# Kernel optimization log

Measured on AMD Instinct MI355X. Metric: run time of the kernel, lower is better.

## Reference

```python
import jax, jax.numpy as jnp
import numpy as np

B, T, D = 4, 2048, 1024
H, KD, VD = 16, 64, 64  # num_heads, key_dim, value_dim; H*KD == D


def setup_inputs() -> dict:
    key = jax.random.key(0)
    ks = jax.random.split(key, 10)
    s = 0.02
    return {
        "q_in": jax.random.normal(ks[0], (B, T, D), jnp.float32),
        "v_in": jax.random.normal(ks[1], (B, T, D), jnp.float32),
        "Wq": jax.random.normal(ks[2], (D, H * KD), jnp.float32) * s,
        "bq": jnp.zeros((H * KD,), jnp.float32),
        "Wk": jax.random.normal(ks[3], (D, H * KD), jnp.float32) * s,
        "bk": jnp.zeros((H * KD,), jnp.float32),
        "Wv": jax.random.normal(ks[4], (D, H * VD), jnp.float32) * s,
        "bv": jnp.zeros((H * VD,), jnp.float32),
        "Wo": jax.random.normal(ks[5], (H * VD, D), jnp.float32) * s,
        "bo": jnp.zeros((D,), jnp.float32),
    }


def reference(q_in, v_in, Wq, bq, Wk, bk, Wv, bv, Wo, bo):
    # QKV projections (key defaults to value input)
    q = q_in @ Wq + bq                      # [B,T,H*KD]
    k = v_in @ Wk + bk                      # [B,T,H*KD]
    v = v_in @ Wv + bv                      # [B,T,H*VD]
    q = q.reshape(B, T, H, KD)
    k = k.reshape(B, T, H, KD)
    v = v.reshape(B, T, H, VD)
    # scaled dot-product attention, scores materialized as [B,H,Tq,Tv]
    q = q / jnp.sqrt(jnp.asarray(KD, q.dtype))
    scores = jnp.einsum('bqnh,bvnh->bnqv', q, k)
    weights = jax.nn.softmax(scores, axis=-1)
    out = jnp.einsum('bnqv,bvnh->bqnh', weights, v)  # [B,Tq,H,VD]
    out = out.reshape(B, T, H * VD)
    return out @ Wo + bo                    # [B,T,D]
```

## Files before the change

### kernel.cpp

```cpp
#include <hip/hip_runtime.h>

#define BATCH  4
#define T_SEQ  2048
#define NH     16
#define DMODEL 1024
#define HD     64

typedef float    f32x4 __attribute__((ext_vector_type(4)));
typedef _Float16 f16x8 __attribute__((ext_vector_type(8)));
typedef _Float16 f16x4 __attribute__((ext_vector_type(4)));
typedef __fp16   h16x2 __attribute__((ext_vector_type(2)));

#define LOG2E 1.44269504088896f

__device__ __forceinline__ void lds_load16(const void* g, void* l) {
  __builtin_amdgcn_global_load_lds((const __attribute__((address_space(1))) void*)g,
                                   (__attribute__((address_space(3))) void*)l, 16, 0, 0);
}

__device__ __forceinline__ f16x4 pack4_f16(float a, float b, float c, float d) {
  union { h16x2 h[2]; f16x4 f; } u;
  u.h[0] = __builtin_amdgcn_cvt_pkrtz(a, b);
  u.h[1] = __builtin_amdgcn_cvt_pkrtz(c, d);
  return u.f;
}

__global__ __launch_bounds__(256) void cast2_f32_to_f16(
    const float* __restrict__ a, const float* __restrict__ bsrc,
    _Float16* __restrict__ oa, _Float16* __restrict__ ob, int n4) {
  const float* in = blockIdx.y ? bsrc : a;
  _Float16* out = blockIdx.y ? ob : oa;
  int i = blockIdx.x * 256 + threadIdx.x;
  if (i < n4) {
    float4 v = ((const float4*)in)[i];
    f16x4 o = { (_Float16)v.x, (_Float16)v.y, (_Float16)v.z, (_Float16)v.w };
    ((f16x4*)out)[i] = o;
  }
}

__global__ __launch_bounds__(256) void transcast_w4(
    const float* __restrict__ W0, const float* __restrict__ W1,
    const float* __restrict__ W2, const float* __restrict__ W3,
    _Float16* __restrict__ T0, _Float16* __restrict__ T1,
    _Float16* __restrict__ T2, _Float16* __restrict__ T3) {
  const float* W; _Float16* Wt;
  switch (blockIdx.z) {
    case 0: W = W0; Wt = T0; break;
    case 1: W = W1; Wt = T1; break;
    case 2: W = W2; Wt = T2; break;
    default: W = W3; Wt = T3; break;
  }
  __shared__ float L[64][65];
  const int n0 = blockIdx.x * 64, k0 = blockIdx.y * 64;
  const int tx = threadIdx.x & 15, ty = threadIdx.x >> 4;
#pragma unroll
  for (int i = 0; i < 4; ++i) {
    float4 v = *(const float4*)&W[(size_t)(k0 + ty + 16 * i) * DMODEL + n0 + tx * 4];
    L[ty + 16 * i][tx * 4 + 0] = v.x;
    L[ty + 16 * i][tx * 4 + 1] = v.y;
    L[ty + 16 * i][tx * 4 + 2] = v.z;
    L[ty + 16 * i][tx * 4 + 3] = v.w;
  }
  __syncthreads();
#pragma unroll
  for (int i = 0; i < 4; ++i) {
    int n = n0 + ty + 16 * i;
    f16x4 o;
#pragma unroll
    for (int j = 0; j < 4; ++j) o[j] = (_Float16)L[tx * 4 + j][ty + 16 * i];
    *(f16x4*)&Wt[(size_t)n * DMODEL + k0 + tx * 4] = o;
  }
}

__device__ __forceinline__ void gemm_body(
    const _Float16* __restrict__ A, const _Float16* __restrict__ Wt,
    const float* __restrict__ bias, void* __restrict__ Cout, float scale,
    int mode, _Float16* As0, _Float16* Bs0, _Float16* As1, _Float16* Bs1) {
  const int K = DMODEL, N = DMODEL;
  const int tid = threadIdx.x, lane = tid & 63, wave = tid >> 6;
  const int bid = blockIdx.x + blockIdx.y * gridDim.x;
  const int m0 = ((bid & 7) * 8 + ((bid >> 3) & 7)) * 128;
  const int n0 = (bid >> 6) * 128;
  const int wm = (wave & 1) * 4, wn = (wave >> 1) * 4;
  const int m16 = lane & 15, quad = lane >> 4;

  const _Float16* ap[4]; const _Float16* bp[4];
#pragma unroll
  for (int i = 0; i < 4; ++i) {
    int gi = wave * 4 + i;
    int row = (gi >> 1) * 16 + m16;
    int kof = (gi & 1) * 32 + quad * 8;
    ap[i] = A  + (size_t)(m0 + row) * K + kof;
    bp[i] = Wt + (size_t)(n0 + row) * K + kof;
  }

  f32x4 acc[4][4] = {};

  auto stage = [&](int k0, _Float16* Asb, _Float16* Bsb) {
#pragma unroll
    for (int i = 0; i < 4; ++i) {
      lds_load16(ap[i] + k0, Asb + (wave * 4 + i) * 512);
      lds_load16(bp[i] + k0, Bsb + (wave * 4 + i) * 512);
    }
  };
  auto compute = [&](const _Float16* Asb, const _Float16* Bsb) {
#pragma unroll
    for (int s = 0; s < 2; ++s) {
      f16x8 af[4], bf[4];
#pragma unroll
      for (int t = 0; t < 4; ++t) {
        af[t] = *(const f16x8*)(Asb + (((wm + t) * 2 + s) * 64 + lane) * 8);
        bf[t] = *(const f16x8*)(Bsb + (((wn + t) * 2 + s) * 64 + lane) * 8);
      }
#pragma unroll
      for (int mi = 0; mi < 4; ++mi)
#pragma unroll
        for (int ni = 0; ni < 4; ++ni)
          acc[mi][ni] = __builtin_amdgcn_mfma_f32_16x16x32_f16(af[mi], bf[ni], acc[mi][ni], 0, 0, 0);
    }
  };

  stage(0, As0, Bs0);
  __syncthreads();
#pragma unroll
  for (int k0 = 0; k0 < 1024; k0 += 128) {
    stage(k0 + 64, As1, Bs1);
    compute(As0, Bs0);
    __syncthreads();
    if (k0 + 128 < 1024) stage(k0 + 128, As0, Bs0);
    compute(As1, Bs1);
    __syncthreads();
  }

  if (mode == 2) {
#pragma unroll
    for (int mi = 0; mi < 4; ++mi)
#pragma unroll
      for (int ni = 0; ni < 4; ++ni) {
        int row = m0 + (wm + mi) * 16 + quad * 4;
        int col = n0 + (wn + ni) * 16 + m16;
        int bb = row >> 11, tt = row & (T_SEQ - 1);
        int hh = col >> 6, dd = col & 63;
        float bv = bias[col];
        f16x4 pv = pack4_f16(acc[mi][ni][0] + bv, acc[mi][ni][1] + bv,
                             acc[mi][ni][2] + bv, acc[mi][ni][3] + bv);
        *(f16x4*)&((_Float16*)Cout)[(((size_t)bb * NH + hh) * HD + dd) * T_SEQ + tt] = pv;
      }
  } else {
#pragma unroll
    for (int mi = 0; mi < 4; ++mi)
#pragma unroll
      for (int r = 0; r < 4; ++r) {
        int row = m0 + (wm + mi) * 16 + quad * 4 + r;
#pragma unroll
        for (int ni = 0; ni < 4; ++ni) {
          int col = n0 + (wn + ni) * 16 + m16;
          float v = (acc[mi][ni][r] + bias[col]) * scale;
          if (mode == 1) ((float*)Cout)[(size_t)row * N + col] = v;
          else           ((_Float16*)Cout)[(size_t)row * N + col] = (_Float16)v;
        }
      }
  }
}

__global__ __launch_bounds__(256) void gemm_qkv(
    const _Float16* __restrict__ Aq, const _Float16* __restrict__ Av,
    const _Float16* __restrict__ Wq, const _Float16* __restrict__ Wk,
    const _Float16* __restrict__ Wv,
    const float* __restrict__ bq, const float* __restrict__ bk,
    const float* __restrict__ bv,
    _Float16* __restrict__ Cq, _Float16* __restrict__ Ck, _Float16* __restrict__ Cv) {
  __shared__ _Float16 As0[128 * 64], Bs0[128 * 64], As1[128 * 64], Bs1[128 * 64];
  const _Float16* A; const _Float16* Wt; const float* bias; _Float16* C;
  float scale; int mode;
  if (blockIdx.z == 0)      { A = Aq; Wt = Wq; bias = bq; C = Cq; scale = 0.125f * LOG2E; mode = 0; }
  else if (blockIdx.z == 1) { A = Av; Wt = Wk; bias = bk; C = Ck; scale = 1.f; mode = 0; }
  else                      { A = Av; Wt = Wv; bias = bv; C = Cv; scale = 1.f; mode = 2; }
  gemm_body(A, Wt, bias, C, scale, mode, As0, Bs0, As1, Bs1);
}

__global__ __launch_bounds__(256) void gemm_out(
    const _Float16* __restrict__ A, const _Float16* __restrict__ Wt,
    const float* __restrict__ bias, float* __restrict__ Cout) {
  __shared__ _Float16 As0[128 * 64], Bs0[128 * 64], As1[128 * 64], Bs1[128 * 64];
  gemm_body(A, Wt, bias, Cout, 1.f, 1, As0, Bs0, As1, Bs1);
}

__global__ __launch_bounds__(256) void attn_mfma(
    const _Float16* __restrict__ Q, const _Float16* __restrict__ Kb,
    const _Float16* __restrict__ Vt, _Float16* __restrict__ O) {
  __shared__ _Float16 Ks0[64 * 64], Vs0[64 * 64], Ks1[64 * 64], Vs1[64 * 64];
  __shared__ _Float16 Ps[4 * 2048];

  const int tid = threadIdx.x, lane = tid & 63, wave = tid >> 6;
  const int m16 = lane & 15, quad = lane >> 4;
  const int bidl = blockIdx.x + 16 * blockIdx.y + 256 * blockIdx.z;
  const int h = bidl & 15;
  const int q0 = ((bidl >> 4) & 15) * 128;
  const int b = bidl >> 8;
  const int wq = wave * 32;
  const int wbase = wave * 2048;

  f16x8 qf[2][2];
#pragma unroll
  for (int mi = 0; mi < 2; ++mi)
#pragma unroll
    for (int ki = 0; ki < 2; ++ki) {
      int q = q0 + wq + mi * 16 + m16;
      qf[mi][ki] = *(const f16x8*)(Q + (((size_t)b * T_SEQ + q) * NH + h) * HD + ki * 32 + quad * 8);
    }

  const _Float16 *kp[2], *vp[2];
#pragma unroll
  for (int i = 0; i < 2; ++i) {
    int g = wave * 128 + i * 64 + lane;
    int tk = (g >> 7) * 16 + (g & 15);
    int dkof = ((g >> 6) & 1) * 32 + ((g >> 4) & 3) * 8;
    kp[i] = Kb + (((size_t)b * T_SEQ + tk) * NH + h) * HD + dkof;
    int dvof = (g >> 7) * 16 + (g & 15);
    int tv = ((g >> 6) & 1) * 32 + ((g >> 4) & 3) * 8;
    vp[i] = Vt + (((size_t)b * NH + h) * HD + dvof) * T_SEQ + tv;
  }

  int pw[2][4];
#pragma unroll
  for (int mi = 0; mi < 2; ++mi)
#pragma unroll
    for (int nt = 0; nt < 4; ++nt) {
      int kt = nt >> 1;
      int q8 = ((nt & 1) << 1) | (quad >> 1);
      pw[mi][nt] = wbase + ((mi * 2 + kt) * 64 + q8 * 16 + m16) * 8 + (quad & 1) * 4;
    }

  const f16x8 onef = {(_Float16)1, (_Float16)1, (_Float16)1, (_Float16)1,
                      (_Float16)1, (_Float16)1, (_Float16)1, (_Float16)1};

  f32x4 o_acc[2][4] = {};
  f32x4 l_acc[2] = {};

  auto stageKV = [&](int kv, _Float16* Kd, _Float16* Vd) {
#pragma unroll
    for (int i = 0; i < 2; ++i) {
      lds_load16(kp[i] + (size_t)kv * (NH * HD), Kd + (wave * 2 + i) * 512);
      lds_load16(vp[i] + kv, Vd + (wave * 2 + i) * 512);
    }
  };

  auto tile = [&](const _Float16* Kd, const _Float16* Vd) {
    f32x4 st[2][4] = {};
#pragma unroll
    for (int nt = 0; nt < 4; ++nt)
#pragma unroll
      for (int ki = 0; ki < 2; ++ki) {
        f16x8 kf = *(const f16x8*)(Kd + ((nt * 2 + ki) * 64 + lane) * 8);
        st[0][nt] = __builtin_amdgcn_mfma_f32_16x16x32_f16(kf, qf[0][ki], st[0][nt], 0, 0, 0);
        st[1][nt] = __builtin_amdgcn_mfma_f32_16x16x32_f16(kf, qf[1][ki], st[1][nt], 0, 0, 0);
      }
#pragma unroll
    for (int mi = 0; mi < 2; ++mi)
#pragma unroll
      for (int nt = 0; nt < 4; ++nt) {
        f16x4 p = pack4_f16(__builtin_amdgcn_exp2f(st[mi][nt][0]),
                            __builtin_amdgcn_exp2f(st[mi][nt][1]),
                            __builtin_amdgcn_exp2f(st[mi][nt][2]),
                            __builtin_amdgcn_exp2f(st[mi][nt][3]));
        *(f16x4*)(Ps + pw[mi][nt]) = p;
      }
#pragma unroll
    for (int kt = 0; kt < 2; ++kt) {
      f16x8 pf0 = *(const f16x8*)(Ps + wbase + ((0 * 2 + kt) * 64 + lane) * 8);
      f16x8 pf1 = *(const f16x8*)(Ps + wbase + ((1 * 2 + kt) * 64 + lane) * 8);
      l_acc[0] = __builtin_amdgcn_mfma_f32_16x16x32_f16(pf0, onef, l_acc[0], 0, 0, 0);
      l_acc[1] = __builtin_amdgcn_mfma_f32_16x16x32_f16(pf1, onef, l_acc[1], 0, 0, 0);
#pragma unroll
      for (int nd = 0; nd < 4; ++nd) {
        f16x8 vf = *(const f16x8*)(Vd + ((nd * 2 + kt) * 64 + lane) * 8);
        o_acc[0][nd] = __builtin_amdgcn_mfma_f32_16x16x32_f16(pf0, vf, o_acc[0][nd], 0, 0, 0);
        o_acc[1][nd] = __builtin_amdgcn_mfma_f32_16x16x32_f16(pf1, vf, o_acc[1][nd], 0, 0, 0);
      }
    }
  };

  stageKV(0, Ks0, Vs0);
  __syncthreads();
  for (int kv = 0; kv < T_SEQ; kv += 128) {
    stageKV(kv + 64, Ks1, Vs1);
    tile(Ks0, Vs0);
    __syncthreads();
    if (kv + 128 < T_SEQ) stageKV(kv + 128, Ks0, Vs0);
    tile(Ks1, Vs1);
    __syncthreads();
  }

#pragma unroll
  for (int mi = 0; mi < 2; ++mi)
#pragma unroll
    for (int r = 0; r < 4; ++r) {
      float inv = 1.f / l_acc[mi][r];
      int q = q0 + wq + mi * 16 + quad * 4 + r;
#pragma unroll
      for (int nd = 0; nd < 4; ++nd) {
        int d = nd * 16 + m16;
        O[(((size_t)b * T_SEQ + q) * NH + h) * HD + d] = (_Float16)(o_acc[mi][nd][r] * inv);
      }
    }
}

extern "C" void kernel_launch(void* const* d_in, const int* in_sizes, int n_in,
                              void* d_out, int out_size, void* d_ws, size_t ws_size,
                              hipStream_t stream) {
  const float* q_in = (const float*)d_in[0];
  const float* v_in = (const float*)d_in[1];
  const float* Wq   = (const float*)d_in[2];
  const float* bq   = (const float*)d_in[3];
  const float* Wk   = (const float*)d_in[4];
  const float* bk   = (const float*)d_in[5];
  const float* Wv   = (const float*)d_in[6];
  const float* bv   = (const float*)d_in[7];
  const float* Wo   = (const float*)d_in[8];
  const float* bo   = (const float*)d_in[9];
  float* out = (float*)d_out;

  const size_t MB = 1u << 20;
  char* ws = (char*)d_ws;
  _Float16* q16  = (_Float16*)(ws);
  _Float16* v16  = (_Float16*)(ws + 16 * MB);
  _Float16* qbuf = (_Float16*)(ws + 32 * MB);
  _Float16* kbuf = (_Float16*)(ws + 48 * MB);
  _Float16* vtb  = (_Float16*)(ws + 64 * MB);
  _Float16* Wqt  = (_Float16*)(ws + 80 * MB);
  _Float16* Wkt  = (_Float16*)(ws + 82 * MB);
  _Float16* Wvt  = (_Float16*)(ws + 84 * MB);
  _Float16* Wot  = (_Float16*)(ws + 86 * MB);

  const int n4 = BATCH * T_SEQ * DMODEL / 4;
  cast2_f32_to_f16<<<dim3(n4 / 256, 2), 256, 0, stream>>>(q_in, v_in, q16, v16, n4);

  transcast_w4<<<dim3(16, 16, 4), 256, 0, stream>>>(Wq, Wk, Wv, Wo, Wqt, Wkt, Wvt, Wot);

  dim3 gg(DMODEL / 128, BATCH * T_SEQ / 128, 3);
  gemm_qkv<<<gg, 256, 0, stream>>>(q16, v16, Wqt, Wkt, Wvt, bq, bk, bv, qbuf, kbuf, vtb);

  attn_mfma<<<dim3(16, 16, 4), 256, 0, stream>>>(qbuf, kbuf, vtb, qbuf);

  gemm_out<<<dim3(8, 64), 256, 0, stream>>>(qbuf, Wot, bo, out);
}
```

Measured before the change: 359.3 us.

## Enlarge GEMM and attention tiles, drop double buffering for single-buffered LDS

The QKV GEMM moves to 256x128 tiles (8x4 MFMA per wave), and attention moves to 256 queries per block (64 per wave). Both reuse each staged K/V or weight tile across more rows, cutting global and LDS traffic per FLOP. All three kernels drop LDS double buffering in favour of a single buffer with two barriers per step, and launch bounds are set to raise occupancy. The trade-off is losing load/compute overlap within a block plus higher register pressure from the larger accumulators, which could cause spills or lower occupancy. Attention also runs only 512 blocks, which fills fewer CUs.

```diff
diff --git a/kernel.cpp b/kernel.cpp
--- a/kernel.cpp
+++ b/kernel.cpp
@@ -72,69 +72,59 @@
   }
 }
 
-__device__ __forceinline__ void gemm_body(
+__device__ __forceinline__ void gemm_big_body(
     const _Float16* __restrict__ A, const _Float16* __restrict__ Wt,
     const float* __restrict__ bias, void* __restrict__ Cout, float scale,
-    int mode, _Float16* As0, _Float16* Bs0, _Float16* As1, _Float16* Bs1) {
-  const int K = DMODEL, N = DMODEL;
-  const int tid = threadIdx.x, lane = tid & 63, wave = tid >> 6;
+    int mode, _Float16* As, _Float16* Bs) {
+  const int K = DMODEL;
+  const int lane = threadIdx.x & 63, wave = threadIdx.x >> 6;
   const int bid = blockIdx.x + blockIdx.y * gridDim.x;
-  const int m0 = ((bid & 7) * 8 + ((bid >> 3) & 7)) * 128;
-  const int n0 = (bid >> 6) * 128;
-  const int wm = (wave & 1) * 4, wn = (wave >> 1) * 4;
+  const int m0 = ((bid & 7) * 4 + ((bid >> 3) & 3)) * 256;
+  const int n0 = (bid >> 5) * 128;
+  const int wm = (wave & 1) * 8;
+  const int wn = (wave >> 1) * 4;
   const int m16 = lane & 15, quad = lane >> 4;
 
-  const _Float16* ap[4]; const _Float16* bp[4];
-#pragma unroll
-  for (int i = 0; i < 4; ++i) {
-    int gi = wave * 4 + i;
-    int row = (gi >> 1) * 16 + m16;
-    int kof = (gi & 1) * 32 + quad * 8;
-    ap[i] = A  + (size_t)(m0 + row) * K + kof;
-    bp[i] = Wt + (size_t)(n0 + row) * K + kof;
-  }
-
-  f32x4 acc[4][4] = {};
-
-  auto stage = [&](int k0, _Float16* Asb, _Float16* Bsb) {
-#pragma unroll
-    for (int i = 0; i < 4; ++i) {
-      lds_load16(ap[i] + k0, Asb + (wave * 4 + i) * 512);
-      lds_load16(bp[i] + k0, Bsb + (wave * 4 + i) * 512);
-    }
-  };
-  auto compute = [&](const _Float16* Asb, const _Float16* Bsb) {
+  const _Float16* ap[8]; const _Float16* bp[4];
+#pragma unroll
+  for (int j = 0; j < 8; ++j) {
+    int g = wave * 8 + j;
+    ap[j] = A + (size_t)(m0 + (g >> 1) * 16 + m16) * K + (g & 1) * 32 + quad * 8;
+  }
+#pragma unroll
+  for (int j = 0; j < 4; ++j) {
+    int g = wave * 4 + j;
+    bp[j] = Wt + (size_t)(n0 + (g >> 1) * 16 + m16) * K + (g & 1) * 32 + quad * 8;
+  }
+
+  f32x4 acc[8][4] = {};
+
+  for (int k0 = 0; k0 < 1024; k0 += 64) {
+    __syncthreads();
+#pragma unroll
+    for (int j = 0; j < 8; ++j) lds_load16(ap[j] + k0, As + (wave * 8 + j) * 512);
+#pragma unroll
+    for (int j = 0; j < 4; ++j) lds_load16(bp[j] + k0, Bs + (wave * 4 + j) * 512);
+    __syncthreads();
 #pragma unroll
     for (int s = 0; s < 2; ++s) {
-      f16x8 af[4], bf[4];
-#pragma unroll
-      for (int t = 0; t < 4; ++t) {
-        af[t] = *(const f16x8*)(Asb + (((wm + t) * 2 + s) * 64 + lane) * 8);
-        bf[t] = *(const f16x8*)(Bsb + (((wn + t) * 2 + s) * 64 + lane) * 8);
-      }
-#pragma unroll
-      for (int mi = 0; mi < 4; ++mi)
+      f16x8 bf[4];
+#pragma unroll
+      for (int t = 0; t < 4; ++t)
+        bf[t] = *(const f16x8*)(Bs + (((wn + t) * 2 + s) * 64 + lane) * 8);
+#pragma unroll
+      for (int mi = 0; mi < 8; ++mi) {
+        f16x8 af = *(const f16x8*)(As + (((wm + mi) * 2 + s) * 64 + lane) * 8);
 #pragma unroll
         for (int ni = 0; ni < 4; ++ni)
-          acc[mi][ni] = __builtin_amdgcn_mfma_f32_16x16x32_f16(af[mi], bf[ni], acc[mi][ni], 0, 0, 0);
-    }
-  };
-
-  stage(0, As0, Bs0);
-  __syncthreads();
-#pragma unroll
-  for (int k0 = 0; k0 < 1024; k0 += 128) {
-    stage(k0 + 64, As1, Bs1);
-    compute(As0, Bs0);
-    __syncthreads();
-    if (k0 + 128 < 1024) stage(k0 + 128, As0, Bs0);
-    compute(As1, Bs1);
-    __syncthreads();
+          acc[mi][ni] = __builtin_amdgcn_mfma_f32_16x16x32_f16(af, bf[ni], acc[mi][ni], 0, 0, 0);
+      }
+    }
   }
 
   if (mode == 2) {
 #pragma unroll
-    for (int mi = 0; mi < 4; ++mi)
+    for (int mi = 0; mi < 8; ++mi)
 #pragma unroll
       for (int ni = 0; ni < 4; ++ni) {
         int row = m0 + (wm + mi) * 16 + quad * 4;
@@ -148,7 +138,7 @@
       }
   } else {
 #pragma unroll
-    for (int mi = 0; mi < 4; ++mi)
+    for (int mi = 0; mi < 8; ++mi)
 #pragma unroll
       for (int r = 0; r < 4; ++r) {
         int row = m0 + (wm + mi) * 16 + quad * 4 + r;
@@ -156,54 +146,107 @@
         for (int ni = 0; ni < 4; ++ni) {
           int col = n0 + (wn + ni) * 16 + m16;
           float v = (acc[mi][ni][r] + bias[col]) * scale;
-          if (mode == 1) ((float*)Cout)[(size_t)row * N + col] = v;
-          else           ((_Float16*)Cout)[(size_t)row * N + col] = (_Float16)v;
+          ((_Float16*)Cout)[(size_t)row * DMODEL + col] = (_Float16)v;
         }
       }
   }
 }
 
-__global__ __launch_bounds__(256) void gemm_qkv(
+__global__ __launch_bounds__(256, 2) void gemm_qkv(
     const _Float16* __restrict__ Aq, const _Float16* __restrict__ Av,
     const _Float16* __restrict__ Wq, const _Float16* __restrict__ Wk,
     const _Float16* __restrict__ Wv,
     const float* __restrict__ bq, const float* __restrict__ bk,
     const float* __restrict__ bv,
     _Float16* __restrict__ Cq, _Float16* __restrict__ Ck, _Float16* __restrict__ Cv) {
-  __shared__ _Float16 As0[128 * 64], Bs0[128 * 64], As1[128 * 64], Bs1[128 * 64];
+  __shared__ _Float16 As[256 * 64];
+  __shared__ _Float16 Bs[128 * 64];
   const _Float16* A; const _Float16* Wt; const float* bias; _Float16* C;
   float scale; int mode;
   if (blockIdx.z == 0)      { A = Aq; Wt = Wq; bias = bq; C = Cq; scale = 0.125f * LOG2E; mode = 0; }
   else if (blockIdx.z == 1) { A = Av; Wt = Wk; bias = bk; C = Ck; scale = 1.f; mode = 0; }
   else                      { A = Av; Wt = Wv; bias = bv; C = Cv; scale = 1.f; mode = 2; }
-  gemm_body(A, Wt, bias, C, scale, mode, As0, Bs0, As1, Bs1);
-}
-
-__global__ __launch_bounds__(256) void gemm_out(
+  gemm_big_body(A, Wt, bias, C, scale, mode, As, Bs);
+}
+
+__global__ __launch_bounds__(256, 3) void gemm_out(
     const _Float16* __restrict__ A, const _Float16* __restrict__ Wt,
     const float* __restrict__ bias, float* __restrict__ Cout) {
-  __shared__ _Float16 As0[128 * 64], Bs0[128 * 64], As1[128 * 64], Bs1[128 * 64];
-  gemm_body(A, Wt, bias, Cout, 1.f, 1, As0, Bs0, As1, Bs1);
-}
-
-__global__ __launch_bounds__(256) void attn_mfma(
+  __shared__ _Float16 As[128 * 64], Bs[128 * 64];
+  const int K = DMODEL;
+  const int lane = threadIdx.x & 63, wave = threadIdx.x >> 6;
+  const int bid = blockIdx.x + blockIdx.y * gridDim.x;
+  const int m0 = ((bid & 7) * 8 + ((bid >> 3) & 7)) * 128;
+  const int n0 = (bid >> 6) * 128;
+  const int wm = (wave & 1) * 4, wn = (wave >> 1) * 4;
+  const int m16 = lane & 15, quad = lane >> 4;
+
+  const _Float16* ap[4]; const _Float16* bp[4];
+#pragma unroll
+  for (int i = 0; i < 4; ++i) {
+    int gi = wave * 4 + i;
+    int row = (gi >> 1) * 16 + m16;
+    int kof = (gi & 1) * 32 + quad * 8;
+    ap[i] = A  + (size_t)(m0 + row) * K + kof;
+    bp[i] = Wt + (size_t)(n0 + row) * K + kof;
+  }
+
+  f32x4 acc[4][4] = {};
+
+  for (int k0 = 0; k0 < 1024; k0 += 64) {
+    __syncthreads();
+#pragma unroll
+    for (int i = 0; i < 4; ++i) {
+      lds_load16(ap[i] + k0, As + (wave * 4 + i) * 512);
+      lds_load16(bp[i] + k0, Bs + (wave * 4 + i) * 512);
+    }
+    __syncthreads();
+#pragma unroll
+    for (int s = 0; s < 2; ++s) {
+      f16x8 af[4], bf[4];
+#pragma unroll
+      for (int t = 0; t < 4; ++t) {
+        af[t] = *(const f16x8*)(As + (((wm + t) * 2 + s) * 64 + lane) * 8);
+        bf[t] = *(const f16x8*)(Bs + (((wn + t) * 2 + s) * 64 + lane) * 8);
+      }
+#pragma unroll
+      for (int mi = 0; mi < 4; ++mi)
+#pragma unroll
+        for (int ni = 0; ni < 4; ++ni)
+          acc[mi][ni] = __builtin_amdgcn_mfma_f32_16x16x32_f16(af[mi], bf[ni], acc[mi][ni], 0, 0, 0);
+    }
+  }
+
+#pragma unroll
+  for (int mi = 0; mi < 4; ++mi)
+#pragma unroll
+    for (int r = 0; r < 4; ++r) {
+      int row = m0 + (wm + mi) * 16 + quad * 4 + r;
+#pragma unroll
+      for (int ni = 0; ni < 4; ++ni) {
+        int col = n0 + (wn + ni) * 16 + m16;
+        Cout[(size_t)row * DMODEL + col] = acc[mi][ni][r] + bias[col];
+      }
+    }
+}
+
+__global__ __launch_bounds__(256, 2) void attn_mfma(
     const _Float16* __restrict__ Q, const _Float16* __restrict__ Kb,
     const _Float16* __restrict__ Vt, _Float16* __restrict__ O) {
-  __shared__ _Float16 Ks0[64 * 64], Vs0[64 * 64], Ks1[64 * 64], Vs1[64 * 64];
-  __shared__ _Float16 Ps[4 * 2048];
-
-  const int tid = threadIdx.x, lane = tid & 63, wave = tid >> 6;
+  __shared__ _Float16 Ks[64 * 64], Vs[64 * 64];
+  __shared__ _Float16 Ps[4 * 4096];
+
+  const int lane = threadIdx.x & 63, wave = threadIdx.x >> 6;
   const int m16 = lane & 15, quad = lane >> 4;
-  const int bidl = blockIdx.x + 16 * blockIdx.y + 256 * blockIdx.z;
-  const int h = bidl & 15;
-  const int q0 = ((bidl >> 4) & 15) * 128;
-  const int b = bidl >> 8;
-  const int wq = wave * 32;
-  const int wbase = wave * 2048;
-
-  f16x8 qf[2][2];
-#pragma unroll
-  for (int mi = 0; mi < 2; ++mi)
+  const int h = blockIdx.x;
+  const int q0 = blockIdx.y * 256;
+  const int b = blockIdx.z;
+  const int wq = wave * 64;
+  const int wbase = wave * 4096;
+
+  f16x8 qf[4][2];
+#pragma unroll
+  for (int mi = 0; mi < 4; ++mi)
 #pragma unroll
     for (int ki = 0; ki < 2; ++ki) {
       int q = q0 + wq + mi * 16 + m16;
@@ -222,9 +265,9 @@
     vp[i] = Vt + (((size_t)b * NH + h) * HD + dvof) * T_SEQ + tv;
   }
 
-  int pw[2][4];
-#pragma unroll
-  for (int mi = 0; mi < 2; ++mi)
+  int pw[4][4];
+#pragma unroll
+  for (int mi = 0; mi < 4; ++mi)
 #pragma unroll
     for (int nt = 0; nt < 4; ++nt) {
       int kt = nt >> 1;
@@ -235,29 +278,31 @@
   const f16x8 onef = {(_Float16)1, (_Float16)1, (_Float16)1, (_Float16)1,
                       (_Float16)1, (_Float16)1, (_Float16)1, (_Float16)1};
 
-  f32x4 o_acc[2][4] = {};
-  f32x4 l_acc[2] = {};
-
-  auto stageKV = [&](int kv, _Float16* Kd, _Float16* Vd) {
+  f32x4 o_acc[4][4] = {};
+  f32x4 l_acc[4] = {};
+
+  for (int kv = 0; kv < T_SEQ; kv += 64) {
+    __syncthreads();
 #pragma unroll
     for (int i = 0; i < 2; ++i) {
-      lds_load16(kp[i] + (size_t)kv * (NH * HD), Kd + (wave * 2 + i) * 512);
-      lds_load16(vp[i] + kv, Vd + (wave * 2 + i) * 512);
-    }
-  };
-
-  auto tile = [&](const _Float16* Kd, const _Float16* Vd) {
-    f32x4 st[2][4] = {};
+      lds_load16(kp[i] + (size_t)kv * (NH * HD), Ks + (wave * 2 + i) * 512);
+      lds_load16(vp[i] + kv, Vs + (wave * 2 + i) * 512);
+    }
+    __syncthreads();
+
+    f32x4 st[4][4] = {};
 #pragma unroll
     for (int nt = 0; nt < 4; ++nt)
 #pragma unroll
       for (int ki = 0; ki < 2; ++ki) {
-        f16x8 kf = *(const f16x8*)(Kd + ((nt * 2 + ki) * 64 + lane) * 8);
-        st[0][nt] = __builtin_amdgcn_mfma_f32_16x16x32_f16(kf, qf[0][ki], st[0][nt], 0, 0, 0);
-        st[1][nt] = __builtin_amdgcn_mfma_f32_16x16x32_f16(kf, qf[1][ki], st[1][nt], 0, 0, 0);
-      }
-#pragma unroll
-    for (int mi = 0; mi < 2; ++mi)
+        f16x8 kf = *(const f16x8*)(Ks + ((nt * 2 + ki) * 64 + lane) * 8);
+#pragma unroll
+        for (int mi = 0; mi < 4; ++mi)
+          st[mi][nt] = __builtin_amdgcn_mfma_f32_16x16x32_f16(kf, qf[mi][ki], st[mi][nt], 0, 0, 0);
+      }
+
+#pragma unroll
+    for (int mi = 0; mi < 4; ++mi)
 #pragma unroll
       for (int nt = 0; nt < 4; ++nt) {
         f16x4 p = pack4_f16(__builtin_amdgcn_exp2f(st[mi][nt][0]),
@@ -266,34 +311,27 @@
                             __builtin_amdgcn_exp2f(st[mi][nt][3]));
         *(f16x4*)(Ps + pw[mi][nt]) = p;
       }
+
 #pragma unroll
     for (int kt = 0; kt < 2; ++kt) {
-      f16x8 pf0 = *(const f16x8*)(Ps + wbase + ((0 * 2 + kt) * 64 + lane) * 8);
-      f16x8 pf1 = *(const f16x8*)(Ps + wbase + ((1 * 2 + kt) * 64 + lane) * 8);
-      l_acc[0] = __builtin_amdgcn_mfma_f32_16x16x32_f16(pf0, onef, l_acc[0], 0, 0, 0);
-      l_acc[1] = __builtin_amdgcn_mfma_f32_16x16x32_f16(pf1, onef, l_acc[1], 0, 0, 0);
+      f16x8 pf[4];
+#pragma unroll
+      for (int mi = 0; mi < 4; ++mi) {
+        pf[mi] = *(const f16x8*)(Ps + wbase + ((mi * 2 + kt) * 64 + lane) * 8);
+        l_acc[mi] = __builtin_amdgcn_mfma_f32_16x16x32_f16(pf[mi], onef, l_acc[mi], 0, 0, 0);
+      }
 #pragma unroll
       for (int nd = 0; nd < 4; ++nd) {
-        f16x8 vf = *(const f16x8*)(Vd + ((nd * 2 + kt) * 64 + lane) * 8);
-        o_acc[0][nd] = __builtin_amdgcn_mfma_f32_16x16x32_f16(pf0, vf, o_acc[0][nd], 0, 0, 0);
-        o_acc[1][nd] = __builtin_amdgcn_mfma_f32_16x16x32_f16(pf1, vf, o_acc[1][nd], 0, 0, 0);
-      }
-    }
-  };
-
-  stageKV(0, Ks0, Vs0);
-  __syncthreads();
-  for (int kv = 0; kv < T_SEQ; kv += 128) {
-    stageKV(kv + 64, Ks1, Vs1);
-    tile(Ks0, Vs0);
-    __syncthreads();
-    if (kv + 128 < T_SEQ) stageKV(kv + 128, Ks0, Vs0);
-    tile(Ks1, Vs1);
-    __syncthreads();
-  }
-
-#pragma unroll
-  for (int mi = 0; mi < 2; ++mi)
+        f16x8 vf = *(const f16x8*)(Vs + ((nd * 2 + kt) * 64 + lane) * 8);
+#pragma unroll
+        for (int mi = 0; mi < 4; ++mi)
+          o_acc[mi][nd] = __builtin_amdgcn_mfma_f32_16x16x32_f16(pf[mi], vf, o_acc[mi][nd], 0, 0, 0);
+      }
+    }
+  }
+
+#pragma unroll
+  for (int mi = 0; mi < 4; ++mi)
 #pragma unroll
     for (int r = 0; r < 4; ++r) {
       float inv = 1.f / l_acc[mi][r];
@@ -338,10 +376,10 @@
 
   transcast_w4<<<dim3(16, 16, 4), 256, 0, stream>>>(Wq, Wk, Wv, Wo, Wqt, Wkt, Wvt, Wot);
 
-  dim3 gg(DMODEL / 128, BATCH * T_SEQ / 128, 3);
-  gemm_qkv<<<gg, 256, 0, stream>>>(q16, v16, Wqt, Wkt, Wvt, bq, bk, bv, qbuf, kbuf, vtb);
-
-  attn_mfma<<<dim3(16, 16, 4), 256, 0, stream>>>(qbuf, kbuf, vtb, qbuf);
+  gemm_qkv<<<dim3(8, 32, 3), 256, 0, stream>>>(q16, v16, Wqt, Wkt, Wvt, bq, bk, bv,
+                                               qbuf, kbuf, vtb);
+
+  attn_mfma<<<dim3(16, 8, 4), 256, 0, stream>>>(qbuf, kbuf, vtb, qbuf);
 
   gemm_out<<<dim3(8, 64), 256, 0, stream>>>(qbuf, Wot, bo, out);
 }
```

Measured after the change: 332.4 us. -7.5%, faster.
